# Kernel tuning notes

Hardware: AMD Instinct MI355X
Metric: run time of the kernel (lower is better)

## Reference

```python
import jax, jax.numpy as jnp
import numpy as np

B = 500_000      # batch rows
F = 100          # fixed by x.view(-1, 100)
NT = 10          # number of tails (clusters)
C = 10           # cluster size (features per tail)
H = 7            # hidden = ceil(0.75 * C)


def setup_inputs() -> dict:
    key = jax.random.key(0)
    ks = jax.random.split(key, 7)
    x = jax.random.normal(ks[0], (B, F), dtype=jnp.float32)
    Wt = jax.random.normal(ks[1], (NT, H, C), dtype=jnp.float32) * 0.1
    hbias_t = jax.random.normal(ks[2], (NT, H), dtype=jnp.float32) * 0.1
    vbias_t = jax.random.normal(ks[3], (NT, C), dtype=jnp.float32) * 0.1
    Wh = jax.random.normal(ks[4], (H, NT), dtype=jnp.float32) * 0.1
    hbias_h = jax.random.normal(ks[5], (H,), dtype=jnp.float32) * 0.1
    vbias_h = jax.random.normal(ks[6], (NT,), dtype=jnp.float32) * 0.1
    clusters = jnp.arange(F, dtype=jnp.int32).reshape(NT, C)
    return {"x": x, "Wt": Wt, "hbias_t": hbias_t, "vbias_t": vbias_t,
            "Wh": Wh, "hbias_h": hbias_h, "vbias_h": vbias_h,
            "clusters": clusters}


def reference(x, Wt, hbias_t, vbias_t, Wh, hbias_h, vbias_h, clusters):
    x = x.reshape(-1, F)
    # fused gather: [B, NT, C]
    xc = x[:, clusters]
    # tail encoders: z = xc @ We.T + hbias  (We = Wt[t], shape [H, C])
    z = jnp.einsum('btc,thc->bth', xc, Wt) + hbias_t[None]          # [B, NT, H]
    # tail decoders (tied weights W.T): out = z @ We + vbias
    out = jnp.einsum('bth,thc->btc', z, Wt) + vbias_t[None]          # [B, NT, C]
    # per-sample, per-tail RMSE then log
    rmse = jnp.sqrt(jnp.mean((out - xc) ** 2, axis=-1))              # [B, NT]
    tails = jnp.log(rmse)                                            # [B, NT]
    # head autoencoder over tail scores
    zh = tails @ Wh.T + hbias_h                                      # [B, H]
    head_out = zh @ Wh + vbias_h                                     # [B, NT]
    return head_out, tails
```

## Files before the change

kernel.cpp:

```cpp
#include <hip/hip_runtime.h>


typedef float v2f __attribute__((ext_vector_type(2)));
typedef float v4f __attribute__((ext_vector_type(4)));

constexpr int F  = 100;
constexpr int NT = 10;
constexpr int C  = 10;
constexpr int H  = 7;
constexpr int BLOCK = 320;
constexpr int RPB   = 64;
constexpr int XSTR  = 102;

__device__ __forceinline__ void do_tile(
    int t,
    float* __restrict__ xrow,
    const float* __restrict__ Wt,
    const float* __restrict__ hbt,
    const float* __restrict__ vbt)
{
    const int cb = t * 10;
    const v2f* __restrict__ xr2 = (const v2f*)(xrow + cb);
    v2f xc[5];
    #pragma unroll
    for (int c2 = 0; c2 < 5; ++c2) xc[c2] = xr2[c2];

    v2f out[5];
    #pragma unroll
    for (int c2 = 0; c2 < 5; ++c2) {
        out[c2].x = vbt[t * C + 2 * c2];
        out[c2].y = vbt[t * C + 2 * c2 + 1];
    }
    #pragma unroll
    for (int h = 0; h < H; ++h) {
        v2f w[5];
        #pragma unroll
        for (int c2 = 0; c2 < 5; ++c2) {
            w[c2].x = Wt[(t * H + h) * C + 2 * c2];
            w[c2].y = Wt[(t * H + h) * C + 2 * c2 + 1];
        }
        v2f za; za.x = hbt[t * H + h]; za.y = 0.f;
        #pragma unroll
        for (int c2 = 0; c2 < 5; ++c2)
            za = __builtin_elementwise_fma(xc[c2], w[c2], za);
        const float z = za.x + za.y;
        v2f zz; zz.x = z; zz.y = z;
        #pragma unroll
        for (int c2 = 0; c2 < 5; ++c2)
            out[c2] = __builtin_elementwise_fma(zz, w[c2], out[c2]);
    }
    v2f a2; a2.x = 0.f; a2.y = 0.f;
    #pragma unroll
    for (int c2 = 0; c2 < 5; ++c2) {
        const v2f d = out[c2] - xc[c2];
        a2 = __builtin_elementwise_fma(d, d, a2);
    }
    const float acc = a2.x + a2.y;
    xrow[cb] = 0.5f * __logf(acc * 0.1f);
}

__global__ __launch_bounds__(BLOCK, 8) void kitnet_main(
    const float* __restrict__ x,
    const float* __restrict__ Wt,
    const float* __restrict__ hbt,
    const float* __restrict__ vbt,
    const float* __restrict__ Wh,
    const float* __restrict__ hbh,
    const float* __restrict__ vbh,
    float* __restrict__ head_out,
    float* __restrict__ tails_out,
    int B)
{
    __shared__ float xs[RPB * XSTR];

    const int tid = threadIdx.x;
    const long long r0 = (long long)blockIdx.x * RPB;
    const int nrows = (int)min((long long)RPB, (long long)B - r0);

    {
        const v4f* __restrict__ xg = (const v4f*)(x + r0 * F);
        const int n4 = nrows * (F / 4);
        #pragma unroll
        for (int k = 0; k < 5; ++k) {
            const int idx = tid + k * BLOCK;
            if (idx < n4) {
                v4f v = __builtin_nontemporal_load(&xg[idx]);
                const int row  = idx / 25;
                const int feat = (idx - row * 25) * 4;
                v2f* d = (v2f*)&xs[row * XSTR + feat];
                v2f lo; lo.x = v.x; lo.y = v.y;
                v2f hi; hi.x = v.z; hi.y = v.w;
                d[0] = lo; d[1] = hi;
            }
        }
    }
    __syncthreads();

    const int lane = tid & 63;
    const int wave = __builtin_amdgcn_readfirstlane(tid >> 6);
    float* xrow = &xs[lane * XSTR];
    if (lane < nrows) {
        do_tile(2 * wave,     xrow, Wt, hbt, vbt);
        do_tile(2 * wave + 1, xrow, Wt, hbt, vbt);
    }
    __syncthreads();

    const int ntask = nrows * 5;
    if (tid < ntask) {
        const int row = tid / 5;
        const int c0  = (tid - row * 5) * 2;
        const float* __restrict__ trow = &xs[row * XSTR];
        float tl[NT];
        #pragma unroll
        for (int t = 0; t < NT; ++t) tl[t] = trow[10 * t];
        float zh[H];
        #pragma unroll
        for (int h = 0; h < H; ++h) {
            float s = hbh[h];
            #pragma unroll
            for (int t = 0; t < NT; ++t) s = fmaf(tl[t], Wh[h * NT + t], s);
            zh[h] = s;
        }
        float h0 = vbh[c0], h1 = vbh[c0 + 1];
        #pragma unroll
        for (int h = 0; h < H; ++h) {
            h0 = fmaf(zh[h], Wh[h * NT + c0],     h0);
            h1 = fmaf(zh[h], Wh[h * NT + c0 + 1], h1);
        }
        const long long o = (r0 + row) * NT + c0;
        v2f hv; hv.x = h0;      hv.y = h1;
        v2f tv; tv.x = tl[c0];  tv.y = tl[c0 + 1];
        *(v2f*)(head_out  + o) = hv;
        *(v2f*)(tails_out + o) = tv;
    }
}

extern "C" void kernel_launch(void* const* d_in, const int* in_sizes, int n_in,
                              void* d_out, int out_size, void* d_ws, size_t ws_size,
                              hipStream_t stream) {
    const float* x   = (const float*)d_in[0];
    const float* Wt  = (const float*)d_in[1];
    const float* hbt = (const float*)d_in[2];
    const float* vbt = (const float*)d_in[3];
    const float* Wh  = (const float*)d_in[4];
    const float* hbh = (const float*)d_in[5];
    const float* vbh = (const float*)d_in[6];
    const int B = in_sizes[0] / F;
    float* head  = (float*)d_out;
    float* tails = head + (size_t)B * NT;
    const int grid = (B + RPB - 1) / RPB;
    kitnet_main<<<grid, BLOCK, 0, stream>>>(x, Wt, hbt, vbt, Wh, hbh, vbh,
                                            head, tails, B);
}
```

Before: 298.7 us.

## Make kernel persistent with double-buffered LDS prefetch of next row tile

Converts the one-tile-per-block kernel into a persistent grid of up to 768 blocks. Each block loops over 64-row tiles and prefetches the next tile's x rows into registers while computing the current tile, then writes them into a second LDS buffer. Block size doubles to 640 threads so each wave handles a single tail instead of two. This is meant to overlap global memory latency with compute and cut launch/tail overhead, at the cost of more registers and LDS per block, which may lower occupancy.

```diff
diff --git a/kernel.cpp b/kernel.cpp
--- a/kernel.cpp
+++ b/kernel.cpp
@@ -8,9 +8,10 @@
 constexpr int NT = 10;
 constexpr int C  = 10;
 constexpr int H  = 7;
-constexpr int BLOCK = 320;
-constexpr int RPB   = 64;
+constexpr int BLOCK = 640;
+constexpr int RPH   = 64;
 constexpr int XSTR  = 102;
+constexpr int LDSF  = RPH * XSTR;
 
 __device__ __forceinline__ void do_tile(
     int t,
@@ -71,67 +72,115 @@
     float* __restrict__ tails_out,
     int B)
 {
-    __shared__ float xs[RPB * XSTR];
-
-    const int tid = threadIdx.x;
-    const long long r0 = (long long)blockIdx.x * RPB;
-    const int nrows = (int)min((long long)RPB, (long long)B - r0);
-
-    {
-        const v4f* __restrict__ xg = (const v4f*)(x + r0 * F);
-        const int n4 = nrows * (F / 4);
-        #pragma unroll
-        for (int k = 0; k < 5; ++k) {
-            const int idx = tid + k * BLOCK;
-            if (idx < n4) {
-                v4f v = __builtin_nontemporal_load(&xg[idx]);
-                const int row  = idx / 25;
-                const int feat = (idx - row * 25) * 4;
-                v2f* d = (v2f*)&xs[row * XSTR + feat];
-                v2f lo; lo.x = v.x; lo.y = v.y;
-                v2f hi; hi.x = v.z; hi.y = v.w;
-                d[0] = lo; d[1] = hi;
-            }
-        }
-    }
-    __syncthreads();
-
+    __shared__ float xs[2][LDSF];
+
+    const int tid  = threadIdx.x;
     const int lane = tid & 63;
     const int wave = __builtin_amdgcn_readfirstlane(tid >> 6);
-    float* xrow = &xs[lane * XSTR];
-    if (lane < nrows) {
-        do_tile(2 * wave,     xrow, Wt, hbt, vbt);
-        do_tile(2 * wave + 1, xrow, Wt, hbt, vbt);
-    }
-    __syncthreads();
-
-    const int ntask = nrows * 5;
-    if (tid < ntask) {
-        const int row = tid / 5;
-        const int c0  = (tid - row * 5) * 2;
-        const float* __restrict__ trow = &xs[row * XSTR];
-        float tl[NT];
-        #pragma unroll
-        for (int t = 0; t < NT; ++t) tl[t] = trow[10 * t];
-        float zh[H];
-        #pragma unroll
-        for (int h = 0; h < H; ++h) {
-            float s = hbh[h];
+
+    const long long nh = ((long long)B + RPH - 1) / RPH;
+    const int G = gridDim.x;
+    long long h = blockIdx.x;
+    if (h >= nh) return;
+
+    const int i0 = tid, i1 = tid + BLOCK;
+    const int i2 = tid + 2 * BLOCK;
+
+    {
+        const int nr = (int)(((long long)B - h * RPH) >= RPH
+                                 ? RPH : ((long long)B - h * RPH));
+        const int n4 = nr * 25;
+        const v4f* __restrict__ g4 = (const v4f*)(x + h * (long long)RPH * F);
+        v4f q0, q1, q2;
+        if (i0 < n4) q0 = __builtin_nontemporal_load(&g4[i0]);
+        if (i1 < n4) q1 = __builtin_nontemporal_load(&g4[i1]);
+        if (i2 < n4) q2 = __builtin_nontemporal_load(&g4[i2]);
+        asm volatile("s_waitcnt vmcnt(0)" ::: "memory");
+        __builtin_amdgcn_sched_barrier(0);
+        #define WRQ(ii, qq) if ((ii) < n4) { \
+            const int row = (ii) / 25, f4 = (ii) - row * 25; \
+            v2f* d = (v2f*)&xs[0][row * XSTR + f4 * 4]; \
+            v2f lo; lo.x = (qq).x; lo.y = (qq).y; \
+            v2f hi; hi.x = (qq).z; hi.y = (qq).w; \
+            d[0] = lo; d[1] = hi; }
+        WRQ(i0, q0) WRQ(i1, q1) WRQ(i2, q2)
+        asm volatile("s_waitcnt lgkmcnt(0)" ::: "memory");
+        __builtin_amdgcn_sched_barrier(0);
+        __builtin_amdgcn_s_barrier();
+    }
+
+    int c = 0;
+    for (; h < nh; h += G, c ^= 1) {
+        const long long hn = h + G;
+        const bool more = hn < nh;
+
+        v4f q0, q1, q2;
+        int n4n = 0;
+        if (more) {
+            const long long remn = (long long)B - hn * RPH;
+            const int nrn = (int)(remn >= RPH ? RPH : remn);
+            n4n = nrn * 25;
+            const v4f* __restrict__ g4 =
+                (const v4f*)(x + hn * (long long)RPH * F);
+            if (i0 < n4n) q0 = __builtin_nontemporal_load(&g4[i0]);
+            if (i1 < n4n) q1 = __builtin_nontemporal_load(&g4[i1]);
+            if (i2 < n4n) q2 = __builtin_nontemporal_load(&g4[i2]);
+        }
+
+        const long long rem = (long long)B - h * RPH;
+        const int nrows = (int)(rem >= RPH ? RPH : rem);
+        if (lane < nrows)
+            do_tile(wave, &xs[c][lane * XSTR], Wt, hbt, vbt);
+
+        asm volatile("s_waitcnt lgkmcnt(0)" ::: "memory");
+        __builtin_amdgcn_sched_barrier(0);
+        __builtin_amdgcn_s_barrier();
+
+        const int ntask = nrows * 5;
+        if (tid < ntask) {
+            const int row = tid / 5;
+            const int c0  = (tid - row * 5) * 2;
+            const float* __restrict__ trow = &xs[c][row * XSTR];
+            float tl[NT];
             #pragma unroll
-            for (int t = 0; t < NT; ++t) s = fmaf(tl[t], Wh[h * NT + t], s);
-            zh[h] = s;
-        }
-        float h0 = vbh[c0], h1 = vbh[c0 + 1];
-        #pragma unroll
-        for (int h = 0; h < H; ++h) {
-            h0 = fmaf(zh[h], Wh[h * NT + c0],     h0);
-            h1 = fmaf(zh[h], Wh[h * NT + c0 + 1], h1);
-        }
-        const long long o = (r0 + row) * NT + c0;
-        v2f hv; hv.x = h0;      hv.y = h1;
-        v2f tv; tv.x = tl[c0];  tv.y = tl[c0 + 1];
-        *(v2f*)(head_out  + o) = hv;
-        *(v2f*)(tails_out + o) = tv;
+            for (int t = 0; t < NT; ++t) tl[t] = trow[10 * t];
+            float zh[H];
+            #pragma unroll
+            for (int hh = 0; hh < H; ++hh) {
+                float s = hbh[hh];
+                #pragma unroll
+                for (int t = 0; t < NT; ++t) s = fmaf(tl[t], Wh[hh * NT + t], s);
+                zh[hh] = s;
+            }
+            float h0 = vbh[c0], h1 = vbh[c0 + 1];
+            #pragma unroll
+            for (int hh = 0; hh < H; ++hh) {
+                h0 = fmaf(zh[hh], Wh[hh * NT + c0],     h0);
+                h1 = fmaf(zh[hh], Wh[hh * NT + c0 + 1], h1);
+            }
+            const long long o = (h * RPH + row) * NT + c0;
+            v2f hv; hv.x = h0;      hv.y = h1;
+            v2f tv; tv.x = tl[c0];  tv.y = tl[c0 + 1];
+            *(v2f*)(head_out  + o) = hv;
+            *(v2f*)(tails_out + o) = tv;
+        }
+
+        if (more) {
+            asm volatile("s_waitcnt vmcnt(0)" ::: "memory");
+            __builtin_amdgcn_sched_barrier(0);
+            const int cn = c ^ 1;
+            #define WRQN(ii, qq) if ((ii) < n4n) { \
+                const int row = (ii) / 25, f4 = (ii) - row * 25; \
+                v2f* d = (v2f*)&xs[cn][row * XSTR + f4 * 4]; \
+                v2f lo; lo.x = (qq).x; lo.y = (qq).y; \
+                v2f hi; hi.x = (qq).z; hi.y = (qq).w; \
+                d[0] = lo; d[1] = hi; }
+            WRQN(i0, q0) WRQN(i1, q1) WRQN(i2, q2)
+        }
+
+        asm volatile("s_waitcnt lgkmcnt(0)" ::: "memory");
+        __builtin_amdgcn_sched_barrier(0);
+        __builtin_amdgcn_s_barrier();
     }
 }
 
@@ -148,7 +197,8 @@
     const int B = in_sizes[0] / F;
     float* head  = (float*)d_out;
     float* tails = head + (size_t)B * NT;
-    const int grid = (B + RPB - 1) / RPB;
+    const long long nh = ((long long)B + RPH - 1) / RPH;
+    const int grid = (int)((nh < 768) ? nh : 768);
     kitnet_main<<<grid, BLOCK, 0, stream>>>(x, Wt, hbt, vbt, Wh, hbh, vbh,
                                             head, tails, B);
 }
```

Result: slower. 335.0 us (+12.2%).
